# Kernel optimization log

Measured on AMD Instinct MI355X. Metric: run time of the kernel, lower is better.

The kernel has to match this reference:

```python
import jax, jax.numpy as jnp
import numpy as np

B, C, D_IN, D_H, D_QK = 64, 512, 1024, 1024, 512
EPS = 1e-5


def setup_inputs() -> dict:
    key = jax.random.key(0)
    ks = jax.random.split(key, 24)
    din2 = D_IN + D_H  # concat([x, h]) feature dim
    s_qk = 1.0 / np.sqrt(din2)
    inp = {
        "x": jax.random.normal(ks[0], (B, C, D_IN), jnp.float32),
        "h": jax.random.normal(ks[1], (B, C, D_H), jnp.float32),
    }
    i = 2
    for g in ("r", "z", "n"):
        inp[f"Wq_{g}"] = jax.random.normal(ks[i], (din2, D_QK), jnp.float32) * s_qk; i += 1
        inp[f"bq_{g}"] = jnp.zeros((D_QK,), jnp.float32)
        inp[f"Wk_{g}"] = jax.random.normal(ks[i], (din2, D_QK), jnp.float32) * s_qk; i += 1
        inp[f"bk_{g}"] = jnp.zeros((D_QK,), jnp.float32)
        inp[f"Wv_{g}"] = jax.random.normal(ks[i], (din2, D_H), jnp.float32) * s_qk; i += 1
        inp[f"bv_{g}"] = jnp.zeros((D_H,), jnp.float32)
    inp["gamma"] = jnp.ones((D_H,), jnp.float32)
    inp["beta"] = jnp.zeros((D_H,), jnp.float32)
    return inp


def _self_attention(xin, Wq, bq, Wk, bk, Wv, bv):
    # xin: (B, C, 2D) ; attention over channel axis C
    Q = xin @ Wq + bq            # (B, C, d_qk)
    K = xin @ Wk + bk            # (B, C, d_qk)
    V = xin @ Wv + bv            # (B, C, d_h)
    scale = 1.0 / jnp.sqrt(jnp.asarray(Q.shape[-1], jnp.float32))
    scores = jnp.einsum("bcd,bed->bce", Q, K) * scale   # (B, C, C)
    attn = jax.nn.softmax(scores, axis=-1)
    return jnp.einsum("bce,bed->bcd", attn, V)          # (B, C, d_h)


def reference(x, h,
              Wq_r, bq_r, Wk_r, bk_r, Wv_r, bv_r,
              Wq_z, bq_z, Wk_z, bk_z, Wv_z, bv_z,
              Wq_n, bq_n, Wk_n, bk_n, Wv_n, bv_n,
              gamma, beta):
    xh = jnp.concatenate([x, h], axis=2)
    r = _self_attention(xh, Wq_r, bq_r, Wk_r, bk_r, Wv_r, bv_r)
    z = _self_attention(xh, Wq_z, bq_z, Wk_z, bk_z, Wv_z, bv_z)
    reset = jax.nn.sigmoid(r)
    update = jax.nn.sigmoid(z)
    xhr = jnp.concatenate([x, h * reset], axis=2)
    n = _self_attention(xhr, Wq_n, bq_n, Wk_n, bk_n, Wv_n, bv_n)
    new_state = (1.0 - update) * h + update * jnp.tanh(n)
    # LayerNorm over last dim
    mu = jnp.mean(new_state, axis=-1, keepdims=True)
    var = jnp.var(new_state, axis=-1, keepdims=True)
    return (new_state - mu) * jax.lax.rsqrt(var + EPS) * gamma + beta
```

## Files before the change

### kernel.cpp

```cpp
#include <hip/hip_runtime.h>
#include <math.h>

typedef __attribute__((ext_vector_type(8))) short short8;
typedef __attribute__((ext_vector_type(4))) float f32x4;

#define EPI_QKV   0
#define EPI_PEXP  1
#define EPI_R     2
#define EPI_Z     3
#define EPI_N     4

__device__ __forceinline__ unsigned short f2bf(float f) {
    unsigned int u = __float_as_uint(f);
    u += 0x7fffu + ((u >> 16) & 1u);
    return (unsigned short)(u >> 16);
}
__device__ __forceinline__ float bf2f(unsigned short s) {
    return __uint_as_float(((unsigned int)s) << 16);
}

struct alignas(8) us4 { unsigned short a, b, c, d; };

#define GLD_LDS16(gp, lp) \
    __builtin_amdgcn_global_load_lds((const __attribute__((address_space(1))) unsigned int*)(gp), \
                                     (__attribute__((address_space(3))) unsigned int*)(lp), 16, 0, 0)

#define BAR   do { asm volatile("" ::: "memory"); __builtin_amdgcn_s_barrier(); \
                   asm volatile("" ::: "memory"); } while (0)
#define VMC6  asm volatile("s_waitcnt vmcnt(6)" ::: "memory")
#define VMC4  asm volatile("s_waitcnt vmcnt(4)" ::: "memory")
#define VMC2  asm volatile("s_waitcnt vmcnt(2)" ::: "memory")
#define VMC0  asm volatile("s_waitcnt vmcnt(0)" ::: "memory")

template<int EPI, int SWZ>
__global__ void __launch_bounds__(512, 2)
gemm256(const unsigned short* __restrict__ A, long long sAb, int lda,
        const unsigned short* __restrict__ Bt, long long sBb, int ldb,
        const float* __restrict__ bias,
        void* __restrict__ C, long long sCb, int ldc,
        int K, float scale,
        const float* __restrict__ hptr,
        const unsigned short* __restrict__ updptr,
        float* __restrict__ psum,
        unsigned short* __restrict__ vt)
{
    extern __shared__ char smem[];

    const int z = blockIdx.z;
    A  += (size_t)z * (size_t)sAb;
    Bt += (size_t)z * (size_t)sBb;

    int bx, by;
    if (SWZ) {
        const int bid = blockIdx.y * 8 + blockIdx.x;
        const int xcd = bid & 7, i = bid >> 3;
        bx = i & 7;
        by = (xcd << 4) | (i >> 3);
    } else {
        bx = blockIdx.x; by = blockIdx.y;
    }
    const int m0 = by * 256;
    const int n0 = bx * 256;

    const int tid = threadIdx.x;
    const int w  = tid >> 6;
    const int l  = tid & 63;
    const int wr = w >> 2;
    const int wc = w & 3;
    const int lr = l & 15;
    const int lg = l >> 4;
    const int rs = (lr & 7) << 4;

    const int srw = l >> 3;
    const int scb = ((l & 7) << 4) ^ (srw << 4);
    const int sbrow = ((w >> 2) << 6) + ((w & 3) << 3);

    const long long ldab = (long long)lda * 2;
    const long long ldbb = (long long)ldb * 2;

    f32x4 acc[2][4][4] = {};
    short8 a0[4][2], a1[4][2], b0[2][2], b1[2][2];

#define STAGE1(gbase, ldbytes, grow0, ldsoff) { \
    const char* g_ = (const char*)(gbase) + \
        (size_t)((grow0) + w*8 + srw) * (ldbytes) + scb; \
    GLD_LDS16(g_, smem + (ldsoff) + (w << 10)); }

#define STAGE1B(gbase, grow0, ldsoff) { \
    const char* g_ = (const char*)(gbase) + \
        (size_t)((grow0) + sbrow + srw) * ldbb + scb; \
    GLD_LDS16(g_, smem + (ldsoff) + (w << 10)); }

#define AOFF(buf) ((buf)*65536)
#define BOFF(buf) ((buf)*65536 + 32768)

#define SA0(buf, base) { STAGE1(base, ldab, m0 + 0,   AOFF(buf) + 0); \
                         STAGE1(base, ldab, m0 + 128, AOFF(buf) + 16384); }
#define SA1(buf, base) { STAGE1(base, ldab, m0 + 64,  AOFF(buf) + 8192); \
                         STAGE1(base, ldab, m0 + 192, AOFF(buf) + 24576); }
#define SB0(buf, base) { STAGE1B(base, n0 + 0,   BOFF(buf) + 0); \
                         STAGE1B(base, n0 + 128, BOFF(buf) + 8192); }
#define SB1(buf, base) { STAGE1B(base, n0 + 32,  BOFF(buf) + 16384); \
                         STAGE1B(base, n0 + 160, BOFF(buf) + 24576); }

#define LDA(dst, MH, buf) { \
    const char* Ab_ = smem + AOFF(buf); \
    _Pragma("unroll") \
    for (int mf = 0; mf < 4; ++mf) { \
        const int row_ = wr*128 + (MH)*64 + mf*16 + lr; \
        _Pragma("unroll") \
        for (int kk = 0; kk < 2; ++kk) \
            dst[mf][kk] = *(const short8*)(Ab_ + row_*128 + ((kk*64 + lg*16) ^ rs)); } }

#define LDB(dst, BH, buf) { \
    const char* Bb_ = smem + BOFF(buf) + (BH)*16384; \
    _Pragma("unroll") \
    for (int nf = 0; nf < 2; ++nf) { \
        const int row_ = wc*32 + nf*16 + lr; \
        _Pragma("unroll") \
        for (int kk = 0; kk < 2; ++kk) \
            dst[nf][kk] = *(const short8*)(Bb_ + row_*128 + ((kk*64 + lg*16) ^ rs)); } }

#define MMA(MH, BH, av, bv) { \
    __builtin_amdgcn_s_setprio(1); \
    _Pragma("unroll") \
    for (int kk = 0; kk < 2; ++kk) \
    _Pragma("unroll") \
    for (int mf = 0; mf < 4; ++mf) \
    _Pragma("unroll") \
    for (int nf = 0; nf < 2; ++nf) \
        acc[MH][mf][(BH)*2+nf] = __builtin_amdgcn_mfma_f32_16x16x32_bf16( \
            av[mf][kk], bv[nf][kk], acc[MH][mf][(BH)*2+nf], 0, 0, 0); \
    __builtin_amdgcn_s_setprio(0); }

    SA0(0, A); SB0(0, Bt); SA1(0, A); SB1(0, Bt);
    SA0(1, A + 64);
    VMC6;
    BAR;
    LDA(a0, 0, 0);
    LDB(b0, 0, 0);

    const int NT = K >> 6;
    for (int t = 0; t < NT; ++t) {
        const int p = t & 1, q = p ^ 1;
        const bool s1 = (t + 1 < NT), s2 = (t + 2 < NT);
        const unsigned short* Anx = A  + (size_t)(t + 1) * 64;
        const unsigned short* Bnx = Bt + (size_t)(t + 1) * 64;
        const unsigned short* Anx2 = A + (size_t)(t + 2) * 64;

        if (t == NT - 1) { VMC0; } else { VMC2; }
        BAR;
        LDB(b1, 1, p);
        if (s1) { SB0(q, Bnx); }
        MMA(0, 0, a0, b0);
        BAR;
        LDA(a1, 1, p);
        if (s1) { SA1(q, Anx); }
        MMA(0, 1, a0, b1);
        VMC4;
        BAR;
        if (s1) { LDA(a0, 0, q); }
        if (s1) { SB1(q, Bnx); }
        MMA(1, 0, a1, b0);
        VMC4;
        BAR;
        if (s1) { LDB(b0, 0, q); }
        if (s2) { SA0(p, Anx2); }
        MMA(1, 1, a1, b1);
    }

    const int Mb = gridDim.y << 8;
    const size_t zc = (size_t)z * (size_t)sCb;

    if (EPI == EPI_PEXP) {
        float psl[2][4][4];
        #pragma unroll
        for (int mh = 0; mh < 2; ++mh)
            #pragma unroll
            for (int mf = 0; mf < 4; ++mf)
                #pragma unroll
                for (int r = 0; r < 4; ++r) psl[mh][mf][r] = 0.0f;

        #pragma unroll
        for (int mh = 0; mh < 2; ++mh)
        #pragma unroll
        for (int mf = 0; mf < 4; ++mf)
        #pragma unroll
        for (int nf = 0; nf < 4; ++nf) {
            const int col = n0 + wc * 64 + nf * 16 + lr;
            #pragma unroll
            for (int r = 0; r < 4; ++r) {
                const int row = m0 + wr * 128 + mh * 64 + mf * 16 + lg * 4 + r;
                const float e = __expf(acc[mh][mf][nf][r] * scale);
                ((unsigned short*)C)[zc + (size_t)row * ldc + col] = f2bf(e);
                psl[mh][mf][r] += e;
            }
        }
        #pragma unroll
        for (int d = 1; d < 16; d <<= 1)
            #pragma unroll
            for (int mh = 0; mh < 2; ++mh)
                #pragma unroll
                for (int mf = 0; mf < 4; ++mf)
                    #pragma unroll
                    for (int r = 0; r < 4; ++r)
                        psl[mh][mf][r] += __shfl_xor(psl[mh][mf][r], d);
        __syncthreads();
        float* red = (float*)smem;
        if (lr == 0) {
            #pragma unroll
            for (int mh = 0; mh < 2; ++mh)
                #pragma unroll
                for (int mf = 0; mf < 4; ++mf)
                    #pragma unroll
                    for (int r = 0; r < 4; ++r)
                        red[wc * 256 + wr * 128 + mh * 64 + mf * 16 + lg * 4 + r]
                            = psl[mh][mf][r];
        }
        __syncthreads();
        if (tid < 256) {
            const float sres = red[tid] + red[256 + tid] + red[512 + tid] + red[768 + tid];
            psum[(size_t)bx * 32768 + (size_t)z * 512 + m0 + tid] = sres;
        }
        return;
    }

    float invs[2][4][4];
    if (EPI == EPI_R || EPI == EPI_Z || EPI == EPI_N) {
        #pragma unroll
        for (int mh = 0; mh < 2; ++mh)
            #pragma unroll
            for (int mf = 0; mf < 4; ++mf)
                #pragma unroll
                for (int r = 0; r < 4; ++r) {
                    const int row = m0 + wr * 128 + mh * 64 + mf * 16 + lg * 4 + r;
                    const size_t gr = (size_t)z * 512 + row;
                    invs[mh][mf][r] = 1.0f / (psum[gr] + psum[32768 + gr]);
                }
    }

    #pragma unroll
    for (int mh = 0; mh < 2; ++mh) {
        #pragma unroll
        for (int mf = 0; mf < 4; ++mf) {
            #pragma unroll
            for (int nf = 0; nf < 4; ++nf) {
                const int col = n0 + wc * 64 + nf * 16 + lr;
                const float bval = (EPI == EPI_QKV) ? bias[col] : 0.0f;
                if (EPI == EPI_QKV && bx >= 4) {
                    const int row0 = m0 + wr * 128 + mh * 64 + mf * 16 + lg * 4;
                    us4 o = { f2bf(acc[mh][mf][nf][0] + bval),
                              f2bf(acc[mh][mf][nf][1] + bval),
                              f2bf(acc[mh][mf][nf][2] + bval),
                              f2bf(acc[mh][mf][nf][3] + bval) };
                    *(us4*)(vt + (size_t)(row0 >> 9) * 524288 +
                            (size_t)(col - 1024) * 512 + (row0 & 511)) = o;
                } else {
                    #pragma unroll
                    for (int r = 0; r < 4; ++r) {
                        const int row = m0 + wr * 128 + mh * 64 + mf * 16 + lg * 4 + r;
                        float v = acc[mh][mf][nf][r] + bval;
                        if (EPI == EPI_QKV) {
                            ((unsigned short*)C)[(size_t)row * ldc + col] = f2bf(v);
                        } else if (EPI == EPI_R) {
                            v *= invs[mh][mf][r];
                            const size_t flat = (size_t)z * Mb + row;
                            const float hh = hptr[flat * 1024 + col];
                            const float sg = 1.0f / (1.0f + __expf(-v));
                            ((unsigned short*)C)[flat * 2048 + 1024 + col] = f2bf(hh * sg);
                        } else if (EPI == EPI_Z) {
                            v *= invs[mh][mf][r];
                            const size_t flat = (size_t)z * Mb + row;
                            const float sg = 1.0f / (1.0f + __expf(-v));
                            ((unsigned short*)C)[flat * 1024 + col] = f2bf(sg);
                        } else {
                            v *= invs[mh][mf][r];
                            const size_t flat = (size_t)z * Mb + row;
                            const float u  = bf2f(updptr[flat * 1024 + col]);
                            const float hh = hptr[flat * 1024 + col];
                            ((float*)C)[flat * 1024 + col] = (1.0f - u) * hh + u * tanhf(v);
                        }
                    }
                }
            }
        }
    }
#undef STAGE1
#undef STAGE1B
#undef AOFF
#undef BOFF
#undef SA0
#undef SA1
#undef SB0
#undef SB1
#undef LDA
#undef LDB
#undef MMA
}


__global__ void __launch_bounds__(256)
prep_xh(const float* __restrict__ x, const float* __restrict__ h, unsigned short* __restrict__ xh)
{
    const size_t t = (size_t)blockIdx.x * 256 + threadIdx.x;
    const size_t f = t * 4;
    const size_t row = f >> 10, col = f & 1023;
    const float4 vx = *(const float4*)(x + f);
    const float4 vh = *(const float4*)(h + f);
    us4 ox = { f2bf(vx.x), f2bf(vx.y), f2bf(vx.z), f2bf(vx.w) };
    us4 oh = { f2bf(vh.x), f2bf(vh.y), f2bf(vh.z), f2bf(vh.w) };
    *(us4*)(xh + row * 2048 + col)        = ox;
    *(us4*)(xh + row * 2048 + 1024 + col) = oh;
}

__global__ void __launch_bounds__(256)
transpose_w(const float* __restrict__ W, unsigned short* __restrict__ WT, int N)
{
    __shared__ float t[32][33];
    const int k0 = blockIdx.y * 32, n0 = blockIdx.x * 32;
    const int tx = threadIdx.x & 31, ty = threadIdx.x >> 5;
    #pragma unroll
    for (int i = 0; i < 4; ++i)
        t[ty + i * 8][tx] = W[(size_t)(k0 + ty + i * 8) * N + n0 + tx];
    __syncthreads();
    #pragma unroll
    for (int i = 0; i < 4; ++i)
        WT[(size_t)(n0 + ty + i * 8) * 2048 + k0 + tx] = f2bf(t[tx][ty + i * 8]);
}

__global__ void __launch_bounds__(256)
layernorm1024(float* __restrict__ Y, const float* __restrict__ gamma, const float* __restrict__ beta)
{
    const int row = blockIdx.x * 4 + (threadIdx.x >> 6);
    const int l = threadIdx.x & 63;
    float* p = Y + (size_t)row * 1024;
    float4 v[4];
    float s = 0.0f, s2 = 0.0f;
    #pragma unroll
    for (int i = 0; i < 4; ++i) {
        v[i] = ((const float4*)p)[i * 64 + l];
        s  += v[i].x + v[i].y + v[i].z + v[i].w;
        s2 += v[i].x * v[i].x + v[i].y * v[i].y + v[i].z * v[i].z + v[i].w * v[i].w;
    }
    #pragma unroll
    for (int d = 32; d; d >>= 1) { s += __shfl_xor(s, d); s2 += __shfl_xor(s2, d); }
    const float mu = s * (1.0f / 1024.0f);
    const float var = s2 * (1.0f / 1024.0f) - mu * mu;
    const float inv = rsqrtf(var + 1e-5f);
    #pragma unroll
    for (int i = 0; i < 4; ++i) {
        const float4 gv = ((const float4*)gamma)[i * 64 + l];
        const float4 bv = ((const float4*)beta)[i * 64 + l];
        float4 o;
        o.x = (v[i].x - mu) * inv * gv.x + bv.x;
        o.y = (v[i].y - mu) * inv * gv.y + bv.y;
        o.z = (v[i].z - mu) * inv * gv.z + bv.z;
        o.w = (v[i].w - mu) * inv * gv.w + bv.w;
        ((float4*)p)[i * 64 + l] = o;
    }
}

__global__ void __launch_bounds__(256)
concat_bias(const float* __restrict__ a, const float* __restrict__ b,
            const float* __restrict__ c, float* __restrict__ o)
{
    const int i = blockIdx.x * 256 + threadIdx.x;
    o[i] = (i < 512) ? a[i] : (i < 1024) ? b[i - 512] : c[i - 1024];
}

extern "C" void kernel_launch(void* const* d_in, const int* in_sizes, int n_in,
                              void* d_out, int out_size, void* d_ws, size_t ws_size,
                              hipStream_t stream)
{
    (void)in_sizes; (void)n_in; (void)out_size; (void)ws_size;

    const float* x = (const float*)d_in[0];
    const float* h = (const float*)d_in[1];
    const float* Wf[9]; const float* bia[9];
    for (int g = 0; g < 3; ++g)
        for (int j = 0; j < 3; ++j) {
            Wf[g * 3 + j]  = (const float*)d_in[2 + g * 6 + j * 2];
            bia[g * 3 + j] = (const float*)d_in[2 + g * 6 + j * 2 + 1];
        }
    const float* gamma = (const float*)d_in[20];
    const float* beta  = (const float*)d_in[21];
    float* out = (float*)d_out;

    const int LDS_BYTES = 131072;
    hipFuncSetAttribute((const void*)gemm256<EPI_QKV, 1>,  hipFuncAttributeMaxDynamicSharedMemorySize, LDS_BYTES);
    hipFuncSetAttribute((const void*)gemm256<EPI_PEXP, 0>, hipFuncAttributeMaxDynamicSharedMemorySize, LDS_BYTES);
    hipFuncSetAttribute((const void*)gemm256<EPI_R, 0>,    hipFuncAttributeMaxDynamicSharedMemorySize, LDS_BYTES);
    hipFuncSetAttribute((const void*)gemm256<EPI_Z, 0>,    hipFuncAttributeMaxDynamicSharedMemorySize, LDS_BYTES);
    hipFuncSetAttribute((const void*)gemm256<EPI_N, 0>,    hipFuncAttributeMaxDynamicSharedMemorySize, LDS_BYTES);

    char* ws = (char*)d_ws;
    size_t off = 0;
    auto alloc = [&](size_t bytes) -> void* {
        void* p = ws + off; off += (bytes + 255) & ~(size_t)255; return p;
    };
    unsigned short* xh  = (unsigned short*)alloc((size_t)32768 * 2048 * 2);
    unsigned short* WT  = (unsigned short*)alloc((size_t)12582912 * 2);
    unsigned short* QK  = (unsigned short*)alloc((size_t)32768 * 1024 * 2);
    unsigned short* Vt  = (unsigned short*)alloc((size_t)32768 * 1024 * 2);
    unsigned short* Pb  = (unsigned short*)alloc((size_t)64 * 512 * 512 * 2);
    unsigned short* upd = (unsigned short*)alloc((size_t)32768 * 1024 * 2);
    float*          psb = (float*)alloc((size_t)2 * 32768 * 4);
    float*          bct = (float*)alloc((size_t)3 * 2048 * 4);

    size_t wtoff[9];
    {
        size_t o = 0;
        for (int g = 0; g < 3; ++g) {
            wtoff[g * 3 + 0] = o; o += (size_t)512 * 2048;
            wtoff[g * 3 + 1] = o; o += (size_t)512 * 2048;
            wtoff[g * 3 + 2] = o; o += (size_t)1024 * 2048;
        }
    }

    prep_xh<<<32768, 256, 0, stream>>>(x, h, xh);
    for (int i = 0; i < 9; ++i) {
        const int N = (i % 3 == 2) ? 1024 : 512;
        transpose_w<<<dim3(N / 32, 64, 1), 256, 0, stream>>>(Wf[i], WT + wtoff[i], N);
    }
    for (int g = 0; g < 3; ++g)
        concat_bias<<<8, 256, 0, stream>>>(bia[g * 3 + 0], bia[g * 3 + 1], bia[g * 3 + 2], bct + g * 2048);

    const float scscale = 0.044194173824159216f;

    auto gate = [&](int g, int epi) {
        const unsigned short* wT = WT + wtoff[g * 3 + 0];
        gemm256<EPI_QKV, 1><<<dim3(8, 128, 1), 512, LDS_BYTES, stream>>>(
            xh, 0, 2048, wT, 0, 2048, bct + g * 2048,
            QK, 0, 1024, 2048, 0.0f, nullptr, nullptr, nullptr, Vt);
        gemm256<EPI_PEXP, 0><<<dim3(2, 2, 64), 512, LDS_BYTES, stream>>>(
            QK, 524288, 1024, QK + 512, 524288, 1024, nullptr,
            Pb, 262144, 512, 512, scscale, nullptr, nullptr, psb, nullptr);
        if (epi == EPI_Z)
            gemm256<EPI_Z, 0><<<dim3(4, 2, 64), 512, LDS_BYTES, stream>>>(
                Pb, 262144, 512, Vt, 524288, 512, nullptr,
                upd, 0, 1024, 512, 0.0f, nullptr, nullptr, psb, nullptr);
        else if (epi == EPI_R)
            gemm256<EPI_R, 0><<<dim3(4, 2, 64), 512, LDS_BYTES, stream>>>(
                Pb, 262144, 512, Vt, 524288, 512, nullptr,
                xh, 0, 2048, 512, 0.0f, h, nullptr, psb, nullptr);
        else
            gemm256<EPI_N, 0><<<dim3(4, 2, 64), 512, LDS_BYTES, stream>>>(
                Pb, 262144, 512, Vt, 524288, 512, nullptr,
                out, 0, 1024, 512, 0.0f, h, upd, psb, nullptr);
    };

    gate(1, EPI_Z);
    gate(0, EPI_R);
    gate(2, EPI_N);
    layernorm1024<<<8192, 256, 0, stream>>>(out, gamma, beta);
}
```

Baseline: 1.323 ms.

## Restructure GEMM main loop to single A register buffer with explicit LDS waits

Reworks the K-loop pipeline of the 256x256 bf16 GEMM. The A fragments are now held in one register set instead of two, and the cross-iteration register prefetch is dropped. LDS reads and global-to-LDS staging are reordered within each iteration, with explicit lgkmcnt waits, sched_barriers and more block barriers. The aim is to cut register pressure (supporting 2 blocks per CU) and tighten synchronisation. In exchange it loses the two-tile-ahead A prefetch and adds barriers, which may expose more LDS and global latency.

```diff
diff --git a/kernel.cpp b/kernel.cpp
--- a/kernel.cpp
+++ b/kernel.cpp
@@ -25,12 +25,13 @@
     __builtin_amdgcn_global_load_lds((const __attribute__((address_space(1))) unsigned int*)(gp), \
                                      (__attribute__((address_space(3))) unsigned int*)(lp), 16, 0, 0)
 
-#define BAR   do { asm volatile("" ::: "memory"); __builtin_amdgcn_s_barrier(); \
-                   asm volatile("" ::: "memory"); } while (0)
-#define VMC6  asm volatile("s_waitcnt vmcnt(6)" ::: "memory")
-#define VMC4  asm volatile("s_waitcnt vmcnt(4)" ::: "memory")
-#define VMC2  asm volatile("s_waitcnt vmcnt(2)" ::: "memory")
-#define VMC0  asm volatile("s_waitcnt vmcnt(0)" ::: "memory")
+#define BAR    __builtin_amdgcn_s_barrier()
+#define LGKM0  do { asm volatile("s_waitcnt lgkmcnt(0)" ::: "memory"); \
+                    __builtin_amdgcn_sched_barrier(0); } while (0)
+#define LGKM8  asm volatile("s_waitcnt lgkmcnt(8)" ::: "memory")
+#define VMC4   asm volatile("s_waitcnt vmcnt(4)" ::: "memory")
+#define VMC2   asm volatile("s_waitcnt vmcnt(2)" ::: "memory")
+#define VMC0   asm volatile("s_waitcnt vmcnt(0)" ::: "memory")
 
 template<int EPI, int SWZ>
 __global__ void __launch_bounds__(512, 2)
@@ -79,7 +80,7 @@
     const long long ldbb = (long long)ldb * 2;
 
     f32x4 acc[2][4][4] = {};
-    short8 a0[4][2], a1[4][2], b0[2][2], b1[2][2];
+    short8 a[4][2], b0[2][2], b1[2][2];
 
 #define STAGE1(gbase, ldbytes, grow0, ldsoff) { \
     const char* g_ = (const char*)(gbase) + \
@@ -103,14 +104,14 @@
 #define SB1(buf, base) { STAGE1B(base, n0 + 32,  BOFF(buf) + 16384); \
                          STAGE1B(base, n0 + 160, BOFF(buf) + 24576); }
 
-#define LDA(dst, MH, buf) { \
+#define LDA8(MH, buf) { \
     const char* Ab_ = smem + AOFF(buf); \
     _Pragma("unroll") \
     for (int mf = 0; mf < 4; ++mf) { \
         const int row_ = wr*128 + (MH)*64 + mf*16 + lr; \
         _Pragma("unroll") \
         for (int kk = 0; kk < 2; ++kk) \
-            dst[mf][kk] = *(const short8*)(Ab_ + row_*128 + ((kk*64 + lg*16) ^ rs)); } }
+            a[mf][kk] = *(const short8*)(Ab_ + row_*128 + ((kk*64 + lg*16) ^ rs)); } }
 
 #define LDB(dst, BH, buf) { \
     const char* Bb_ = smem + BOFF(buf) + (BH)*16384; \
@@ -121,7 +122,7 @@
         for (int kk = 0; kk < 2; ++kk) \
             dst[nf][kk] = *(const short8*)(Bb_ + row_*128 + ((kk*64 + lg*16) ^ rs)); } }
 
-#define MMA(MH, BH, av, bv) { \
+#define MMA16(MH, BH, bv) { \
     __builtin_amdgcn_s_setprio(1); \
     _Pragma("unroll") \
     for (int kk = 0; kk < 2; ++kk) \
@@ -130,43 +131,41 @@
     _Pragma("unroll") \
     for (int nf = 0; nf < 2; ++nf) \
         acc[MH][mf][(BH)*2+nf] = __builtin_amdgcn_mfma_f32_16x16x32_bf16( \
-            av[mf][kk], bv[nf][kk], acc[MH][mf][(BH)*2+nf], 0, 0, 0); \
+            a[mf][kk], bv[nf][kk], acc[MH][mf][(BH)*2+nf], 0, 0, 0); \
     __builtin_amdgcn_s_setprio(0); }
 
     SA0(0, A); SB0(0, Bt); SA1(0, A); SB1(0, Bt);
-    SA0(1, A + 64);
-    VMC6;
+    VMC0;
     BAR;
-    LDA(a0, 0, 0);
-    LDB(b0, 0, 0);
 
     const int NT = K >> 6;
     for (int t = 0; t < NT; ++t) {
         const int p = t & 1, q = p ^ 1;
-        const bool s1 = (t + 1 < NT), s2 = (t + 2 < NT);
-        const unsigned short* Anx = A  + (size_t)(t + 1) * 64;
-        const unsigned short* Bnx = Bt + (size_t)(t + 1) * 64;
-        const unsigned short* Anx2 = A + (size_t)(t + 2) * 64;
-
+        const bool s1 = (t + 1 < NT);
+        const unsigned short* An = A  + (size_t)(t + 1) * 64;
+        const unsigned short* Bn = Bt + (size_t)(t + 1) * 64;
+
+        LDA8(0, p); LDB(b0, 0, p);
+        if (s1) { SB0(q, Bn); }
+        LGKM8;
+        BAR; LGKM0;
+        MMA16(0, 0, b0);
         if (t == NT - 1) { VMC0; } else { VMC2; }
         BAR;
         LDB(b1, 1, p);
-        if (s1) { SB0(q, Bnx); }
-        MMA(0, 0, a0, b0);
+        if (s1) { SA0(q, An); }
+        BAR; LGKM0;
+        MMA16(0, 1, b1);
         BAR;
-        LDA(a1, 1, p);
-        if (s1) { SA1(q, Anx); }
-        MMA(0, 1, a0, b1);
-        VMC4;
+        LDA8(1, p);
+        if (s1) { SA1(q, An); }
+        BAR; LGKM0;
+        MMA16(1, 0, b0);
         BAR;
-        if (s1) { LDA(a0, 0, q); }
-        if (s1) { SB1(q, Bnx); }
-        MMA(1, 0, a1, b0);
-        VMC4;
+        if (s1) { SB1(q, Bn); VMC4; }
         BAR;
-        if (s1) { LDB(b0, 0, q); }
-        if (s2) { SA0(p, Anx2); }
-        MMA(1, 1, a1, b1);
+        MMA16(1, 1, b1);
+        BAR;
     }
 
     const int Mb = gridDim.y << 8;
@@ -293,9 +292,9 @@
 #undef SA1
 #undef SB0
 #undef SB1
-#undef LDA
+#undef LDA8
 #undef LDB
-#undef MMA
+#undef MMA16
 }
 
 
```

Result: no change. 1.342 ms (+1.5%).
